# Kernel optimization log

Hardware: AMD Instinct MI355X
Metric: run time of the kernel (lower is better)

Reference implementation:

```python
import jax, jax.numpy as jnp
import numpy as np

X_DIM = Y_DIM = 512      # render resolution (create_coords x_dim, y_dim)
X_MAX = Y_MAX = 512      # grid extents (== x_mode, y_mode)
Z_DIM = 64
Z_MIN, Z_MAX = 0.0, 1.0
FEATS = 32
BATCH = 8


def _make_coords(x_dim, y_dim, x_max, y_max):
    # Faithful replica of G_Tensor3D.create_coords (incl. half_dx used for ys start).
    half_dx, half_dy = 0.5 / x_dim, 0.5 / y_dim
    xs = np.linspace(half_dx, 1 - half_dx, x_dim, dtype=np.float32)
    ys = np.linspace(half_dx, 1 - half_dy, y_dim, dtype=np.float32)
    xv, yv = np.meshgrid(xs, ys, indexing='ij')
    xy = np.stack((yv.ravel(), xv.ravel()), axis=1)              # [N, 2]
    s = xy * np.array([x_max, y_max], dtype=np.float32)          # scaled coords
    idx = s.astype(np.int64)
    x0 = np.clip(idx[:, 0], 0, x_max - 1)
    y0 = np.clip(idx[:, 1], 0, y_max - 1)
    x1 = np.minimum(x0 + 1, x_max - 1)
    y1 = np.minimum(y0 + 1, y_max - 1)
    lerp = (s - idx.astype(np.float32)).astype(np.float32)       # [N, 2]
    return x0.astype(np.int32), y0.astype(np.int32), x1.astype(np.int32), y1.astype(np.int32), lerp


def setup_inputs() -> dict:
    key = jax.random.key(0)
    kz, kd, kzd, k1, k2, k3, kb1, kb2, kb3 = jax.random.split(key, 9)
    x0, y0, x1, y1, lerp = _make_coords(X_DIM, Y_DIM, X_MAX, Y_MAX)
    return {
        "z": jax.random.uniform(kz, (BATCH,), dtype=jnp.float32, minval=Z_MIN, maxval=Z_MAX),
        "data": 0.0002 * jax.random.normal(kd, (X_MAX, Y_MAX, FEATS), dtype=jnp.float32),
        "z_data": jax.random.normal(kzd, (Z_DIM, FEATS), dtype=jnp.float32),
        "lerp_weights": jnp.asarray(lerp),
        "x0": jnp.asarray(x0), "y0": jnp.asarray(y0),
        "x1": jnp.asarray(x1), "y1": jnp.asarray(y1),
        "W1": 0.1 * jax.random.normal(k1, (FEATS, 32), dtype=jnp.float32),
        "b1": 0.1 * jax.random.normal(kb1, (32,), dtype=jnp.float32),
        "W2": 0.1 * jax.random.normal(k2, (32, 32), dtype=jnp.float32),
        "b2": 0.1 * jax.random.normal(kb2, (32,), dtype=jnp.float32),
        "W3": 0.1 * jax.random.normal(k3, (32, 1), dtype=jnp.float32),
        "b3": 0.1 * jax.random.normal(kb3, (1,), dtype=jnp.float32),
    }


def reference(z, data, z_data, lerp_weights, x0, y0, x1, y1, W1, b1, W2, b2, W3, b3):
    b = z.shape[0]
    # --- z interpolation (torch .long() truncates; z >= 0 here) ---
    zn = (Z_DIM - 1) * (z - Z_MIN) / (Z_MAX - Z_MIN)
    z0i = jnp.clip(zn.astype(jnp.int32), 0, Z_DIM - 1)
    z1i = jnp.minimum(z0i + 1, Z_DIM - 1)
    zl = (zn - jnp.trunc(zn))[:, None]                           # [b, 1]
    z_feat = z_data[z0i] * (1.0 - zl) + z_data[z1i] * zl         # [b, F]
    # --- bilinear spatial gather (note data indexed [y, x] as in source) ---
    wx = lerp_weights[:, 0:1]
    wy = lerp_weights[:, 1:2]
    xy_feat = (data[y0, x0] * (1.0 - wx) * (1.0 - wy)
               + data[y0, x1] * wx * (1.0 - wy)
               + data[y1, x0] * (1.0 - wx) * wy
               + data[y1, x1] * wx * wy)                          # [N, F]
    # --- outer broadcast product + tiny MLP ---
    feat = xy_feat[None, :, :] * z_feat[:, None, :]              # [b, N, F]
    h = jax.nn.relu(feat @ W1 + b1)
    h = jax.nn.relu(h @ W2 + b2)
    out = h @ W3 + b3                                            # [b, N, 1]
    return out.reshape(b, 1, X_DIM, Y_DIM)
```

## Files before the change

### kernel.cpp

```cpp
#include <hip/hip_runtime.h>


typedef float f32x4 __attribute__((ext_vector_type(4)));
typedef short bf16x8 __attribute__((ext_vector_type(8)));

constexpr int NPIX = 512 * 512;
constexpr int PPB  = 64;

union FragU { unsigned int u[4]; uint4 v; bf16x8 s; };

__device__ __forceinline__ unsigned int pack_top16(float e0, float e1) {
    return __builtin_amdgcn_perm(__float_as_uint(e1), __float_as_uint(e0), 0x07060302u);
}
__device__ __forceinline__ float trunc_bf16(float x) {
    return __uint_as_float(__float_as_uint(x) & 0xFFFF0000u);
}

__global__ __launch_bounds__(256) void field_mlp_mfma3(
    const float* __restrict__ z,
    const float* __restrict__ data,
    const float* __restrict__ z_data,
    const float* __restrict__ lerp_w,
    const int* __restrict__ x0a, const int* __restrict__ y0a,
    const int* __restrict__ x1a, const int* __restrict__ y1a,
    const float* __restrict__ W1, const float* __restrict__ b1,
    const float* __restrict__ W2, const float* __restrict__ b2,
    const float* __restrict__ W3, const float* __restrict__ b3,
    float* __restrict__ out)
{
    __shared__ float f_T[PPB][36];
    __shared__ float zf_lds[8][36];
    __shared__ float bias_lds[2][36];
    __shared__ float w3_lds[36];
    __shared__ __align__(16) unsigned int wt_lds[4][32][20];

    const int tid = threadIdx.x;

    {
        const int b = tid >> 5, i = tid & 31;
        const float zn = 63.0f * z[b];
        int z0 = (int)zn; z0 = max(0, min(z0, 63));
        const int z1i = min(z0 + 1, 63);
        const float zl = zn - truncf(zn);
        zf_lds[b][i] = z_data[z0 * 32 + i] * (1.0f - zl) + z_data[z1i * 32 + i] * zl;
    }
    if (tid < 32) {
        bias_lds[0][tid] = b1[tid];
        bias_lds[1][tid] = b2[tid];
        w3_lds[tid]      = W3[tid];
    }
#pragma unroll
    for (int u = 0; u < 2; ++u) {
        const int unit = tid + u * 256;
        const int pxl = unit >> 3, ch = unit & 7;
        const int p = blockIdx.x * PPB + pxl;
        const int ix0 = x0a[p], iy0 = y0a[p], ix1 = x1a[p], iy1 = y1a[p];
        const float2 w2 = *(const float2*)(lerp_w + 2 * p);
        const float wx = w2.x, wy = w2.y;
        const float w00 = (1.0f - wx) * (1.0f - wy);
        const float w01 = wx * (1.0f - wy);
        const float w10 = (1.0f - wx) * wy;
        const float w11 = wx * wy;
        const f32x4* base = (const f32x4*)data;
        const f32x4 c00 = base[(iy0 * 512 + ix0) * 8 + ch];
        const f32x4 c01 = base[(iy0 * 512 + ix1) * 8 + ch];
        const f32x4 c10 = base[(iy1 * 512 + ix0) * 8 + ch];
        const f32x4 c11 = base[(iy1 * 512 + ix1) * 8 + ch];
        const f32x4 v = c00 * w00 + c01 * w01 + c10 * w10 + c11 * w11;
        *(f32x4*)&f_T[pxl][ch * 4] = v;
    }
    {
        const int n = tid & 31, kc = (tid >> 5) * 4, kw = (tid >> 5) * 2;
#pragma unroll
        for (int m = 0; m < 2; ++m) {
            const float* Wm = m ? W2 : W1;
            const float x0 = Wm[(kc + 0) * 32 + n];
            const float x1 = Wm[(kc + 1) * 32 + n];
            const float x2 = Wm[(kc + 2) * 32 + n];
            const float x3 = Wm[(kc + 3) * 32 + n];
            wt_lds[2 * m][n][kw]     = pack_top16(x0, x1);
            wt_lds[2 * m][n][kw + 1] = pack_top16(x2, x3);
            wt_lds[2 * m + 1][n][kw]     = pack_top16(x0 - trunc_bf16(x0), x1 - trunc_bf16(x1));
            wt_lds[2 * m + 1][n][kw + 1] = pack_top16(x2 - trunc_bf16(x2), x3 - trunc_bf16(x3));
        }
    }
    __syncthreads();

    const int l  = tid & 63, w = tid >> 6;
    const int lg = l >> 4,  lr = l & 15;
    const int srow = ((lr >> 2) << 3) + (lr & 3);

    FragU W1f[2][2], W2f[2][2];
#pragma unroll
    for (int t = 0; t < 2; ++t) {
        W1f[t][0].v = *(const uint4*)&wt_lds[0][srow + 4 * t][lg * 4];
        W1f[t][1].v = *(const uint4*)&wt_lds[1][srow + 4 * t][lg * 4];
        W2f[t][0].v = *(const uint4*)&wt_lds[2][t * 16 + lr][lg * 4];
        W2f[t][1].v = *(const uint4*)&wt_lds[3][t * 16 + lr][lg * 4];
    }
    f32x4 zva[2], zvb[2], b1v[2], b2v[2], w3v[2];
#pragma unroll
    for (int bb = 0; bb < 2; ++bb) {
        zva[bb] = *(const f32x4*)&zf_lds[2 * w + bb][lg * 8];
        zvb[bb] = *(const f32x4*)&zf_lds[2 * w + bb][lg * 8 + 4];
    }
#pragma unroll
    for (int t = 0; t < 2; ++t) {
        b1v[t] = *(const f32x4*)&bias_lds[0][8 * lg + 4 * t];
        b2v[t] = *(const f32x4*)&bias_lds[1][t * 16 + 4 * lg];
        w3v[t] = *(const f32x4*)&w3_lds[t * 16 + 4 * lg];
    }
    const float b3s = b3[0];
    const f32x4 vzero = {0.0f, 0.0f, 0.0f, 0.0f};
    float* const outp = out + blockIdx.x * PPB;

#pragma unroll
    for (int pxg = 0; pxg < 4; ++pxg) {
        const int px = pxg * 16 + lr;
        const f32x4 ff0 = *(const f32x4*)&f_T[px][lg * 8];
        const f32x4 ff1 = *(const f32x4*)&f_T[px][lg * 8 + 4];
#pragma unroll
        for (int bb = 0; bb < 2; ++bb) {
            const f32x4 ea = ff0 * zva[bb];
            const f32x4 eb = ff1 * zvb[bb];
            FragU Eh;
            Eh.u[0] = pack_top16(ea[0], ea[1]);
            Eh.u[1] = pack_top16(ea[2], ea[3]);
            Eh.u[2] = pack_top16(eb[0], eb[1]);
            Eh.u[3] = pack_top16(eb[2], eb[3]);
            f32x4 hv[2];
#pragma unroll
            for (int t = 0; t < 2; ++t) {
                f32x4 a = __builtin_amdgcn_mfma_f32_16x16x32_bf16(W1f[t][1].s, Eh.s, vzero, 0, 0, 0);
                a = __builtin_amdgcn_mfma_f32_16x16x32_bf16(W1f[t][0].s, Eh.s, a, 0, 0, 0);
                a = a + b1v[t];
#pragma unroll
                for (int r = 0; r < 4; ++r) a[r] = fmaxf(a[r], 0.0f);
                hv[t] = a;
            }
            FragU Hh, Hl;
            Hh.u[0] = pack_top16(hv[0][0], hv[0][1]);
            Hh.u[1] = pack_top16(hv[0][2], hv[0][3]);
            Hh.u[2] = pack_top16(hv[1][0], hv[1][1]);
            Hh.u[3] = pack_top16(hv[1][2], hv[1][3]);
            f32x4 hl0 = hv[0], hl1 = hv[1];
#pragma unroll
            for (int r = 0; r < 4; ++r) {
                hl0[r] -= trunc_bf16(hv[0][r]);
                hl1[r] -= trunc_bf16(hv[1][r]);
            }
            Hl.u[0] = pack_top16(hl0[0], hl0[1]);
            Hl.u[1] = pack_top16(hl0[2], hl0[3]);
            Hl.u[2] = pack_top16(hl1[0], hl1[1]);
            Hl.u[3] = pack_top16(hl1[2], hl1[3]);
            float o = 0.0f;
#pragma unroll
            for (int t = 0; t < 2; ++t) {
                f32x4 a = __builtin_amdgcn_mfma_f32_16x16x32_bf16(W2f[t][0].s, Hl.s, vzero, 0, 0, 0);
                a = __builtin_amdgcn_mfma_f32_16x16x32_bf16(W2f[t][1].s, Hh.s, a, 0, 0, 0);
                a = __builtin_amdgcn_mfma_f32_16x16x32_bf16(W2f[t][0].s, Hh.s, a, 0, 0, 0);
                a = a + b2v[t];
#pragma unroll
                for (int r = 0; r < 4; ++r)
                    o = fmaf(fmaxf(a[r], 0.0f), w3v[t][r], o);
            }
            o += __shfl_xor(o, 16);
            o += __shfl_xor(o, 32);
            o += b3s;
            if (l < 16)
                __builtin_nontemporal_store(o, outp + (2 * w + bb) * NPIX + px);
        }
    }
}

extern "C" void kernel_launch(void* const* d_in, const int* in_sizes, int n_in,
                              void* d_out, int out_size, void* d_ws, size_t ws_size,
                              hipStream_t stream) {
    const float* zp      = (const float*)d_in[0];
    const float* data    = (const float*)d_in[1];
    const float* z_data  = (const float*)d_in[2];
    const float* lerp_w  = (const float*)d_in[3];
    const int*   x0      = (const int*)d_in[4];
    const int*   y0      = (const int*)d_in[5];
    const int*   x1      = (const int*)d_in[6];
    const int*   y1      = (const int*)d_in[7];
    const float* W1      = (const float*)d_in[8];
    const float* b1      = (const float*)d_in[9];
    const float* W2      = (const float*)d_in[10];
    const float* b2      = (const float*)d_in[11];
    const float* W3      = (const float*)d_in[12];
    const float* b3      = (const float*)d_in[13];
    float* out = (float*)d_out;

    dim3 grid(NPIX / PPB);
    dim3 block(256);
    hipLaunchKernelGGL(field_mlp_mfma3, grid, block, 0, stream,
                       zp, data, z_data, lerp_w, x0, y0, x1, y1,
                       W1, b1, W2, b2, W3, b3, out);
}
```

Before: 128.7 us.

## Process two pixel tiles per block with double-buffered gather prefetch

Each block now handles two 64-pixel tiles instead of one. The bilinear gather for the second tile is issued into registers while the MFMA MLP runs on the first tile, then written to a second LDS buffer. This is meant to hide global gather latency behind compute and to spread the per-block weight and z setup over more pixels. In exchange the grid has half as many blocks and each thread holds more registers, which may reduce occupancy.

```diff
diff --git a/kernel.cpp b/kernel.cpp
--- a/kernel.cpp
+++ b/kernel.cpp
@@ -5,7 +5,8 @@
 typedef short bf16x8 __attribute__((ext_vector_type(8)));
 
 constexpr int NPIX = 512 * 512;
-constexpr int PPB  = 64;
+constexpr int PPT  = 64;
+constexpr int TPB  = 2;
 
 union FragU { unsigned int u[4]; uint4 v; bf16x8 s; };
 
@@ -16,7 +17,7 @@
     return __uint_as_float(__float_as_uint(x) & 0xFFFF0000u);
 }
 
-__global__ __launch_bounds__(256) void field_mlp_mfma3(
+__global__ __launch_bounds__(256) void field_mlp_mfma4(
     const float* __restrict__ z,
     const float* __restrict__ data,
     const float* __restrict__ z_data,
@@ -28,7 +29,7 @@
     const float* __restrict__ W3, const float* __restrict__ b3,
     float* __restrict__ out)
 {
-    __shared__ float f_T[PPB][36];
+    __shared__ float f_T[2][PPT][36];
     __shared__ float zf_lds[8][36];
     __shared__ float bias_lds[2][36];
     __shared__ float w3_lds[36];
@@ -48,26 +49,6 @@
         bias_lds[0][tid] = b1[tid];
         bias_lds[1][tid] = b2[tid];
         w3_lds[tid]      = W3[tid];
-    }
-#pragma unroll
-    for (int u = 0; u < 2; ++u) {
-        const int unit = tid + u * 256;
-        const int pxl = unit >> 3, ch = unit & 7;
-        const int p = blockIdx.x * PPB + pxl;
-        const int ix0 = x0a[p], iy0 = y0a[p], ix1 = x1a[p], iy1 = y1a[p];
-        const float2 w2 = *(const float2*)(lerp_w + 2 * p);
-        const float wx = w2.x, wy = w2.y;
-        const float w00 = (1.0f - wx) * (1.0f - wy);
-        const float w01 = wx * (1.0f - wy);
-        const float w10 = (1.0f - wx) * wy;
-        const float w11 = wx * wy;
-        const f32x4* base = (const f32x4*)data;
-        const f32x4 c00 = base[(iy0 * 512 + ix0) * 8 + ch];
-        const f32x4 c01 = base[(iy0 * 512 + ix1) * 8 + ch];
-        const f32x4 c10 = base[(iy1 * 512 + ix0) * 8 + ch];
-        const f32x4 c11 = base[(iy1 * 512 + ix1) * 8 + ch];
-        const f32x4 v = c00 * w00 + c01 * w01 + c10 * w10 + c11 * w11;
-        *(f32x4*)&f_T[pxl][ch * 4] = v;
     }
     {
         const int n = tid & 31, kc = (tid >> 5) * 4, kw = (tid >> 5) * 2;
@@ -84,6 +65,51 @@
             wt_lds[2 * m + 1][n][kw + 1] = pack_top16(x2 - trunc_bf16(x2), x3 - trunc_bf16(x3));
         }
     }
+
+    int   coff[2][4];
+    float cw[2][4];
+    f32x4 creg[2][4];
+
+    auto tile_idx = [&](int tile) {
+        const int pbase = blockIdx.x * (TPB * PPT) + tile * PPT;
+#pragma unroll
+        for (int u = 0; u < 2; ++u) {
+            const int unit = tid + u * 256;
+            const int pxl = unit >> 3, ch = unit & 7;
+            const int p = pbase + pxl;
+            const int ix0 = x0a[p], iy0 = y0a[p], ix1 = x1a[p], iy1 = y1a[p];
+            const float2 w2 = *(const float2*)(lerp_w + 2 * p);
+            const float wx = w2.x, wy = w2.y;
+            cw[u][0] = (1.0f - wx) * (1.0f - wy);
+            cw[u][1] = wx * (1.0f - wy);
+            cw[u][2] = (1.0f - wx) * wy;
+            cw[u][3] = wx * wy;
+            coff[u][0] = (iy0 * 512 + ix0) * 8 + ch;
+            coff[u][1] = (iy0 * 512 + ix1) * 8 + ch;
+            coff[u][2] = (iy1 * 512 + ix0) * 8 + ch;
+            coff[u][3] = (iy1 * 512 + ix1) * 8 + ch;
+        }
+    };
+    auto tile_corners = [&]() {
+        const f32x4* base = (const f32x4*)data;
+#pragma unroll
+        for (int u = 0; u < 2; ++u)
+#pragma unroll
+            for (int c = 0; c < 4; ++c) creg[u][c] = base[coff[u][c]];
+    };
+    auto tile_write = [&](int buf) {
+#pragma unroll
+        for (int u = 0; u < 2; ++u) {
+            const int unit = tid + u * 256;
+            const int pxl = unit >> 3, ch = unit & 7;
+            const f32x4 v = creg[u][0] * cw[u][0] + creg[u][1] * cw[u][1]
+                          + creg[u][2] * cw[u][2] + creg[u][3] * cw[u][3];
+            *(f32x4*)&f_T[buf][pxl][ch * 4] = v;
+        }
+    };
+
+    tile_idx(0);
+    tile_corners();
     __syncthreads();
 
     const int l  = tid & 63, w = tid >> 6;
@@ -112,13 +138,14 @@
     }
     const float b3s = b3[0];
     const f32x4 vzero = {0.0f, 0.0f, 0.0f, 0.0f};
-    float* const outp = out + blockIdx.x * PPB;
-
-#pragma unroll
-    for (int pxg = 0; pxg < 4; ++pxg) {
+
+    tile_write(0);
+    __syncthreads();
+
+    auto compute_quarter = [&](int buf, int pxg, int obase) {
         const int px = pxg * 16 + lr;
-        const f32x4 ff0 = *(const f32x4*)&f_T[px][lg * 8];
-        const f32x4 ff1 = *(const f32x4*)&f_T[px][lg * 8 + 4];
+        const f32x4 ff0 = *(const f32x4*)&f_T[buf][px][lg * 8];
+        const f32x4 ff1 = *(const f32x4*)&f_T[buf][px][lg * 8 + 4];
 #pragma unroll
         for (int bb = 0; bb < 2; ++bb) {
             const f32x4 ea = ff0 * zva[bb];
@@ -168,7 +195,22 @@
             o += __shfl_xor(o, 32);
             o += b3s;
             if (l < 16)
-                __builtin_nontemporal_store(o, outp + (2 * w + bb) * NPIX + px);
+                __builtin_nontemporal_store(o, out + (2 * w + bb) * NPIX + obase + px);
+        }
+    };
+
+#pragma unroll
+    for (int t = 0; t < TPB; ++t) {
+        const int obase = blockIdx.x * (TPB * PPT) + t * PPT;
+        if (t + 1 < TPB) tile_idx(t + 1);
+        compute_quarter(t & 1, 0, obase);
+        compute_quarter(t & 1, 1, obase);
+        if (t + 1 < TPB) tile_corners();
+        compute_quarter(t & 1, 2, obase);
+        compute_quarter(t & 1, 3, obase);
+        if (t + 1 < TPB) {
+            tile_write((t + 1) & 1);
+            __syncthreads();
         }
     }
 }
@@ -192,9 +234,9 @@
     const float* b3      = (const float*)d_in[13];
     float* out = (float*)d_out;
 
-    dim3 grid(NPIX / PPB);
+    dim3 grid(NPIX / (TPB * PPT));
     dim3 block(256);
-    hipLaunchKernelGGL(field_mlp_mfma3, grid, block, 0, stream,
+    hipLaunchKernelGGL(field_mlp_mfma4, grid, block, 0, stream,
                        zp, data, z_data, lerp_w, x0, y0, x1, y1,
                        W1, b1, W2, b2, W3, b3, out);
 }
```

Result: no change. 130.8 us (+1.6%).
